# Optimization experiments

Hardware: AMD Instinct MI355X
Metric: run time of the kernel (lower is better)

## Reference

```python
import jax, jax.numpy as jnp
import numpy as np

B, L, D, K, NFFT = 4, 8192, 768, 24, 16384


def setup_inputs() -> dict:
    key = jax.random.key(0)
    k1, k2, k3, k4 = jax.random.split(key, 4)
    x = jax.random.normal(k1, (B, L, D), dtype=jnp.float32)
    phi = jax.random.normal(k2, (L, K), dtype=jnp.float32) * 0.1
    M_inputs = jax.random.normal(k3, (D, D), dtype=jnp.float32) * 0.02
    M_filters = jax.random.normal(k4, (K, D), dtype=jnp.float32) * 0.02
    return {"x": x, "phi": phi, "M_inputs": M_inputs, "M_filters": M_filters, "n": NFFT}


def _convolve_approx(u, v, n):
    # u: (B, L, D) projected inputs; v: (L, D) projected filters (per-channel kernels)
    bsz, seq_len, d = u.shape
    sgn = jnp.where(jnp.arange(seq_len) % 2 == 0, 1.0, -1.0).astype(u.dtype)[None, :, None]  # (1,L,1)
    V = jnp.fft.rfft(v.astype(jnp.float32), n=n, axis=0)[None, :, :, None]  # (1,F,D,1)
    U = jnp.stack([u, u * sgn], axis=-1).astype(jnp.float32)  # (B,L,D,2): [plus, sign-flipped]
    Uf = jnp.fft.rfft(U, n=n, axis=1)  # (B,F,D,2)
    conv = jnp.fft.irfft(V * Uf, n=n, axis=1)[:, :seq_len]  # (B,L,D,2)
    U_plus = conv[..., 0]
    U_minus = conv[..., 1] * sgn
    return U_plus, U_minus


def reference(x, phi, M_inputs, M_filters, n):
    x_proj = x @ M_inputs          # (B,L,D)
    phi_proj = phi @ M_filters     # (L,D)
    spectral_plus, spectral_minus = _convolve_approx(x_proj, phi_proj, n)
    return spectral_plus + spectral_minus
```

## Files before the change

kernel.cpp:

```cpp
#include <hip/hip_runtime.h>
#include <stdint.h>

#define B_SZ 4
#define L_SEQ 8192
#define D_CH 768
#define K_F 24
#define NFFT2 8192
#define LDS_BYTES 69632

typedef __attribute__((ext_vector_type(4))) float f32x4;
typedef __attribute__((ext_vector_type(8))) __bf16 bf16x8;

__device__ __forceinline__ uint32_t f2bf1(float f) {
  uint32_t u = __float_as_uint(f);
  return (u + 0x7fffu + ((u >> 16) & 1u)) >> 16;
}
__device__ __forceinline__ uint32_t packbf2(float lo, float hi) {
  return f2bf1(lo) | (f2bf1(hi) << 16);
}
__device__ __forceinline__ float2 unpackbf2(uint32_t v) {
  return float2{__uint_as_float(v << 16), __uint_as_float(v & 0xffff0000u)};
}
__device__ __forceinline__ float2 cmulf(float2 a, float2 b) {
  return float2{a.x * b.x - a.y * b.y, a.x * b.y + a.y * b.x};
}
__device__ __forceinline__ uint32_t pkbf(float lo, float hi) {
  uint32_t r;
  asm("v_cvt_pk_bf16_f32 %0, %1, %2" : "=v"(r) : "v"(lo), "v"(hi));
  return r;
}

__global__ __launch_bounds__(256) void k_mit(const float* __restrict__ Mi,
                                             uint16_t* __restrict__ MiT) {
  int i = blockIdx.x * 256 + threadIdx.x;
  int n = i / 768, e = i - n * 768;
  MiT[i] = (uint16_t)f2bf1(Mi[e * 768 + n]);
}

template <int S>
__device__ __forceinline__ void dft8(float2* x) {
  const float C = 0.70710678118654752f;
  float2 t0{x[0].x + x[4].x, x[0].y + x[4].y}, t1{x[0].x - x[4].x, x[0].y - x[4].y};
  float2 t2{x[2].x + x[6].x, x[2].y + x[6].y}, t3{x[2].x - x[6].x, x[2].y - x[6].y};
  float2 t4{x[1].x + x[5].x, x[1].y + x[5].y}, t5{x[1].x - x[5].x, x[1].y - x[5].y};
  float2 t6{x[3].x + x[7].x, x[3].y + x[7].y}, t7{x[3].x - x[7].x, x[3].y - x[7].y};
  float2 t3r = (S < 0) ? float2{t3.y, -t3.x} : float2{-t3.y, t3.x};
  float2 t7r = (S < 0) ? float2{t7.y, -t7.x} : float2{-t7.y, t7.x};
  float2 e0{t0.x + t2.x, t0.y + t2.y}, e2{t0.x - t2.x, t0.y - t2.y};
  float2 e1{t1.x + t3r.x, t1.y + t3r.y}, e3{t1.x - t3r.x, t1.y - t3r.y};
  float2 o0{t4.x + t6.x, t4.y + t6.y}, o2{t4.x - t6.x, t4.y - t6.y};
  float2 o1{t5.x + t7r.x, t5.y + t7r.y}, o3{t5.x - t7r.x, t5.y - t7r.y};
  float2 o1r = (S < 0) ? float2{C * (o1.x + o1.y), C * (o1.y - o1.x)}
                       : float2{C * (o1.x - o1.y), C * (o1.y + o1.x)};
  float2 o2r = (S < 0) ? float2{o2.y, -o2.x} : float2{-o2.y, o2.x};
  float2 o3r = (S < 0) ? float2{C * (o3.y - o3.x), -C * (o3.x + o3.y)}
                       : float2{-C * (o3.x + o3.y), C * (o3.x - o3.y)};
  x[0] = float2{e0.x + o0.x, e0.y + o0.y};
  x[4] = float2{e0.x - o0.x, e0.y - o0.y};
  x[1] = float2{e1.x + o1r.x, e1.y + o1r.y};
  x[5] = float2{e1.x - o1r.x, e1.y - o1r.y};
  x[2] = float2{e2.x + o2r.x, e2.y + o2r.y};
  x[6] = float2{e2.x - o2r.x, e2.y - o2r.y};
  x[3] = float2{e3.x + o3r.x, e3.y + o3r.y};
  x[7] = float2{e3.x - o3r.x, e3.y - o3r.y};
}

template <int LH, int S, int NT>
__device__ __forceinline__ void pass_r8(float2* a, int tid) {
  constexpr int h = 1 << LH;
  constexpr int st = h + (h >> 4);
  const float ang = (S < 0 ? -6.2831853071795864769f : 6.2831853071795864769f) / (float)(h * 8);
  __syncthreads();
#pragma unroll
  for (int jj = 0; jj < 1024 / NT; ++jj) {
    int j = jj * NT + tid;
    int pos = j & (h - 1);
    int base = ((j >> LH) << (LH + 3)) + pos;
    float2* p = a + (base + (base >> 4));
    float2 x[8];
#pragma unroll
    for (int q = 0; q < 8; ++q) x[q] = p[q * st];
    float sn, cs;
    __sincosf(ang * (float)pos, &sn, &cs);
    float2 w{cs, sn};
    if constexpr (S < 0) {
      dft8<-1>(x);
      float2 wq = w;
      x[1] = cmulf(x[1], wq);
#pragma unroll
      for (int q = 2; q < 8; ++q) {
        wq = cmulf(wq, w);
        x[q] = cmulf(x[q], wq);
      }
    } else {
      float2 wq = w;
      x[1] = cmulf(x[1], wq);
#pragma unroll
      for (int q = 2; q < 8; ++q) {
        wq = cmulf(wq, w);
        x[q] = cmulf(x[q], wq);
      }
      dft8<1>(x);
    }
#pragma unroll
    for (int q = 0; q < 8; ++q) p[q * st] = x[q];
  }
}

__device__ __forceinline__ void p1_fused(float2* a, const uint32_t* __restrict__ row32, int tid) {
#pragma unroll
  for (int jj = 0; jj < 2; ++jj) {
    int j = jj * 512 + tid;
    float2 x[8];
#pragma unroll
    for (int q = 0; q < 4; ++q) x[q] = unpackbf2(row32[j + q * 1024]);
    x[4] = x[5] = x[6] = x[7] = float2{0.f, 0.f};
    dft8<-1>(x);
    float sn, cs;
    __sincosf(-6.2831853071795864769f / 8192.0f * (float)j, &sn, &cs);
    float2 w{cs, sn}, wq = w;
    x[1] = cmulf(x[1], wq);
#pragma unroll
    for (int q = 2; q < 8; ++q) {
      wq = cmulf(wq, w);
      x[q] = cmulf(x[q], wq);
    }
    float2* p = a + (j + (j >> 4));
#pragma unroll
    for (int q = 0; q < 8; ++q) p[q * 1088] = x[q];
  }
}

__device__ __forceinline__ void mid_fused(float2* a, const uint32_t* __restrict__ wrow, int tid) {
  __syncthreads();
#pragma unroll
  for (int jj = 0; jj < 8; ++jj) {
    int j = jj * 512 + tid;
    float2* p = a + (2 * j + ((2 * j) >> 4));
    float2 u = p[0], v = p[1];
    float2 s{u.x + v.x, u.y + v.y}, dd{u.x - v.x, u.y - v.y};
    uint2 wv = *(const uint2*)(wrow + 2 * j);
    s = cmulf(s, unpackbf2(wv.x));
    dd = cmulf(dd, unpackbf2(wv.y));
    p[0] = float2{s.x + dd.x, s.y + dd.y};
    p[1] = float2{s.x - dd.x, s.y - dd.y};
  }
}

__device__ __forceinline__ void last_fused(float2* a, uint32_t* __restrict__ out32, int tid) {
  __syncthreads();
#pragma unroll
  for (int jj = 0; jj < 2; ++jj) {
    int j = jj * 512 + tid;
    float2* p = a + (j + (j >> 4));
    float2 x[8];
#pragma unroll
    for (int q = 0; q < 8; ++q) x[q] = p[q * 1088];
    float sn, cs;
    __sincosf(6.2831853071795864769f / 8192.0f * (float)j, &sn, &cs);
    float2 w{cs, sn}, wq = w;
    x[1] = cmulf(x[1], wq);
#pragma unroll
    for (int q = 2; q < 8; ++q) {
      wq = cmulf(wq, w);
      x[q] = cmulf(x[q], wq);
    }
    dft8<1>(x);
#pragma unroll
    for (int q = 0; q < 4; ++q) out32[j + q * 1024] = packbf2(x[q].x, x[q].y);
  }
}

__global__ __launch_bounds__(256) void k_phi(const float* __restrict__ phi,
                                             float2* __restrict__ Phi2) {
  extern __shared__ float2 buf[];
  int k = blockIdx.x, tid = threadIdx.x;
  const float scale = 2.0f / 8192.0f;
  for (int r = tid; r < 4096; r += 256) {
    buf[r + (r >> 4)] = float2{phi[(2 * r) * K_F + k] * scale, 0.0f};
    int r2i = r + 4096;
    buf[r2i + (r2i >> 4)] = float2{0.0f, 0.0f};
  }
  pass_r8<10, -1, 256>(buf, tid);
  pass_r8<7, -1, 256>(buf, tid);
  pass_r8<4, -1, 256>(buf, tid);
  pass_r8<1, -1, 256>(buf, tid);
  __syncthreads();
  for (int j = tid; j < 4096; j += 256) {
    float2* p = buf + (2 * j + ((2 * j) >> 4));
    float2 u = p[0], v = p[1];
    p[0] = float2{u.x + v.x, u.y + v.y};
    p[1] = float2{u.x - v.x, u.y - v.y};
  }
  __syncthreads();
  for (int f = tid; f < NFFT2; f += 256) Phi2[k * NFFT2 + f] = buf[f + (f >> 4)];
}

__global__ __launch_bounds__(256) void k_w2(const float2* __restrict__ Phi2,
                                            const float* __restrict__ Mf,
                                            uint32_t* __restrict__ W2) {
  __shared__ float2 p[K_F][256];
  __shared__ float mf[K_F][32];
  int tid = threadIdx.x;
  int fc = blockIdx.x & 31, dc = blockIdx.x >> 5;
  int f0 = fc * 256, d0 = dc * 32;
  for (int i = tid; i < K_F * 256; i += 256) {
    int k = i >> 8, fl = i & 255;
    p[k][fl] = Phi2[k * NFFT2 + f0 + fl];
  }
  for (int i = tid; i < K_F * 32; i += 256) {
    int k = i >> 5, dl = i & 31;
    mf[k][dl] = Mf[k * D_CH + d0 + dl];
  }
  __syncthreads();
  for (int dl = 0; dl < 32; ++dl) {
    float re = 0.f, im = 0.f;
#pragma unroll
    for (int k = 0; k < K_F; ++k) {
      float m = mf[k][dl];
      re += m * p[k][tid].x;
      im += m * p[k][tid].y;
    }
    W2[(size_t)(d0 + dl) * NFFT2 + f0 + tid] = packbf2(re, im);
  }
}

__device__ __forceinline__ void gload_lds16(const void* g, void* l) {
  __builtin_amdgcn_global_load_lds(
      (const __attribute__((address_space(1))) void*)g,
      (__attribute__((address_space(3))) void*)l, 16, 0, 0);
}

__global__ __launch_bounds__(256) void k_gemm(const float* __restrict__ X,
                                              const uint16_t* __restrict__ MiT,
                                              uint16_t* __restrict__ Cp) {
  __shared__ uint16_t As[128 * 64];
  __shared__ uint16_t Bs[128 * 64];
  int tid = threadIdx.x;
  int lane = tid & 63, wid = tid >> 6;
  int bm = blockIdx.x / 6, bn = blockIdx.x % 6;
  int m0 = bm * 128, n0 = bn * 128;
  int wr = wid >> 1, wc = wid & 1;
  int lm = lane & 15, lg = lane >> 4;
  f32x4 acc[4][4] = {};

  for (int kt = 0; kt < 12; ++kt) {
    int k0 = kt * 64;
    __syncthreads();
#pragma unroll
    for (int it = 0; it < 4; ++it) {
      int s = it * 256 + tid;
      int row = s >> 3;
      int cb = ((s & 7) << 4) ^ ((row & 7) << 4);
      gload_lds16(MiT + (size_t)(n0 + row) * 768 + k0 + (cb >> 1),
                  (char*)Bs + (it * 256 + wid * 64) * 16);
    }
#pragma unroll
    for (int it = 0; it < 4; ++it) {
      int s = it * 256 + tid;
      int row = s >> 3, c16 = s & 7;
      const float* src = X + (size_t)(m0 + row) * 768 + k0 + c16 * 8;
      float4 f0 = *(const float4*)src;
      float4 f1 = *(const float4*)(src + 4);
      uint4 o;
      o.x = pkbf(f0.x, f0.y);
      o.y = pkbf(f0.z, f0.w);
      o.z = pkbf(f1.x, f1.y);
      o.w = pkbf(f1.z, f1.w);
      *(uint4*)((char*)As + row * 128 + ((c16 << 4) ^ ((row & 7) << 4))) = o;
    }
    asm volatile("s_waitcnt vmcnt(0)" ::: "memory");
    __syncthreads();
#pragma unroll
    for (int ks = 0; ks < 2; ++ks) {
      int kbyte = (ks * 32 + lg * 8) * 2;
      bf16x8 a[4], b[4];
#pragma unroll
      for (int mi = 0; mi < 4; ++mi) {
        int row = wr * 64 + mi * 16 + lm;
        a[mi] = *(const bf16x8*)((const char*)As + row * 128 + (kbyte ^ ((row & 7) << 4)));
      }
#pragma unroll
      for (int ni = 0; ni < 4; ++ni) {
        int row = wc * 64 + ni * 16 + lm;
        b[ni] = *(const bf16x8*)((const char*)Bs + row * 128 + (kbyte ^ ((row & 7) << 4)));
      }
#pragma unroll
      for (int mi = 0; mi < 4; ++mi)
#pragma unroll
        for (int ni = 0; ni < 4; ++ni)
          acc[mi][ni] = __builtin_amdgcn_mfma_f32_16x16x32_bf16(a[mi], b[ni], acc[mi][ni], 0, 0, 0);
    }
  }
#pragma unroll
  for (int mi = 0; mi < 4; ++mi) {
#pragma unroll
    for (int ni = 0; ni < 4; ++ni) {
      int mg = m0 + wr * 64 + mi * 16 + lg * 4;
      int dd = n0 + wc * 64 + ni * 16 + lm;
      int bb = mg >> 13, t = mg & 8191;
      f32x4 v = acc[mi][ni];
      uint2 o;
      o.x = packbf2(v[0], v[1]);
      o.y = packbf2(v[2], v[3]);
      *(uint2*)(Cp + ((size_t)bb * 768 + dd) * 8192 + t) = o;
    }
  }
}

__global__ __launch_bounds__(512, 4) void k_conv(const uint16_t* __restrict__ xprojT,
                                                 const uint32_t* __restrict__ W2,
                                                 uint16_t* __restrict__ convo) {
  extern __shared__ float2 buf[];
  int tid = threadIdx.x;
  int bd = blockIdx.x;
  int d = bd % 768;
  const uint32_t* row32 = (const uint32_t*)(xprojT + (size_t)bd * 8192);
  p1_fused(buf, row32, tid);
  pass_r8<7, -1, 512>(buf, tid);
  pass_r8<4, -1, 512>(buf, tid);
  pass_r8<1, -1, 512>(buf, tid);
  mid_fused(buf, W2 + (size_t)d * NFFT2, tid);
  pass_r8<1, 1, 512>(buf, tid);
  pass_r8<4, 1, 512>(buf, tid);
  pass_r8<7, 1, 512>(buf, tid);
  last_fused(buf, (uint32_t*)(convo + (size_t)bd * 8192), tid);
}

__global__ __launch_bounds__(256) void k_tr(const uint16_t* __restrict__ convo,
                                            float* __restrict__ out) {
  __shared__ uint16_t tile[64][72];
  int tid = threadIdx.x;
  int bx = blockIdx.x;
  int b = bx / 1536;
  int r = bx - b * 1536;
  int d0 = (r >> 7) << 6;
  int t0 = (r & 127) << 6;
  {
    int rr = tid >> 3;
    int c8 = (tid & 7) << 3;
#pragma unroll
    for (int p = 0; p < 2; ++p) {
      int row = p * 32 + rr;
      uint4 v = *(const uint4*)(convo + ((size_t)(b * 768 + d0 + row)) * 8192 + t0 + c8);
      *(uint4*)&tile[row][c8] = v;
    }
  }
  __syncthreads();
  {
    int c4 = (tid & 15) << 2;
    int tg = tid >> 4;
#pragma unroll
    for (int p = 0; p < 4; ++p) {
      int tt = p * 16 + tg;
      float4 o;
      o.x = __uint_as_float((uint32_t)tile[c4 + 0][tt] << 16);
      o.y = __uint_as_float((uint32_t)tile[c4 + 1][tt] << 16);
      o.z = __uint_as_float((uint32_t)tile[c4 + 2][tt] << 16);
      o.w = __uint_as_float((uint32_t)tile[c4 + 3][tt] << 16);
      *(float4*)(out + ((size_t)b * 8192 + t0 + tt) * 768 + d0 + c4) = o;
    }
  }
}

extern "C" void kernel_launch(void* const* d_in, const int* in_sizes, int n_in,
                              void* d_out, int out_size, void* d_ws, size_t ws_size,
                              hipStream_t stream) {
  const float* x   = (const float*)d_in[0];
  const float* phi = (const float*)d_in[1];
  const float* Mi  = (const float*)d_in[2];
  const float* Mf  = (const float*)d_in[3];
  float* out = (float*)d_out;

  uint16_t* xprojT = (uint16_t*)d_out + 25165824;

  char* ws = (char*)d_ws;
  uint16_t* convo = (uint16_t*)ws;
  uint32_t* W2    = (uint32_t*)(ws + 50331648);
  float2*   Phi2  = (float2*)(ws + 75497472);
  uint16_t* MiT   = (uint16_t*)(ws + 77070336);

  k_mit<<<2304, 256, 0, stream>>>(Mi, MiT);
  k_phi<<<24, 256, LDS_BYTES, stream>>>(phi, Phi2);
  k_w2<<<768, 256, 0, stream>>>(Phi2, Mf, W2);
  k_gemm<<<1536, 256, 0, stream>>>(x, MiT, xprojT);
  k_conv<<<3072, 512, LDS_BYTES, stream>>>(xprojT, W2, convo);
  k_tr<<<6144, 256, 0, stream>>>(convo, out);
}
```

Measured before the change: 253.2 us.

## Double-buffer GEMM LDS tiles and remap block indices across XCDs

The projection GEMM now uses two LDS buffers for the A and B tiles. The next K-slice's global loads (A into registers, B via direct-to-LDS loads) are issued before the MFMA work on the current slice, and A is converted and written after that work. This aims to hide global-load latency behind compute and leaves one barrier per iteration instead of two. The block index is also permuted so that consecutive tiles are spread across XCDs in groups, for better L2 locality. The cost is twice the LDS per block, which may lower occupancy, and the in-loop wait on the async B loads relies only on implicit ordering of the vmcnt counter.

```diff
diff --git a/kernel.cpp b/kernel.cpp
--- a/kernel.cpp
+++ b/kernel.cpp
@@ -234,43 +234,60 @@
 __global__ __launch_bounds__(256) void k_gemm(const float* __restrict__ X,
                                               const uint16_t* __restrict__ MiT,
                                               uint16_t* __restrict__ Cp) {
-  __shared__ uint16_t As[128 * 64];
-  __shared__ uint16_t Bs[128 * 64];
+  __shared__ uint16_t As[2][128 * 64];
+  __shared__ uint16_t Bs[2][128 * 64];
   int tid = threadIdx.x;
   int lane = tid & 63, wid = tid >> 6;
-  int bm = blockIdx.x / 6, bn = blockIdx.x % 6;
+  int p = blockIdx.x;
+  int v = (p & 7) * 192 + (p >> 3);
+  int bm = v / 6, bn = v % 6;
   int m0 = bm * 128, n0 = bn * 128;
   int wr = wid >> 1, wc = wid & 1;
   int lm = lane & 15, lg = lane >> 4;
   f32x4 acc[4][4] = {};
-
+  float4 fa[8];
+
+#define LOAD_A(k0)                                                       \
+  _Pragma("unroll") for (int it = 0; it < 4; ++it) {                     \
+    int s = it * 256 + tid;                                              \
+    int row = s >> 3, c16 = s & 7;                                       \
+    const float* src = X + (size_t)(m0 + row) * 768 + (k0) + c16 * 8;    \
+    fa[2 * it] = *(const float4*)src;                                    \
+    fa[2 * it + 1] = *(const float4*)(src + 4);                          \
+  }
+#define STAGE_B(buf, k0)                                                 \
+  _Pragma("unroll") for (int it = 0; it < 4; ++it) {                     \
+    int s = it * 256 + tid;                                              \
+    int row = s >> 3;                                                    \
+    int cb = ((s & 7) << 4) ^ ((row & 7) << 4);                          \
+    gload_lds16(MiT + (size_t)(n0 + row) * 768 + (k0) + (cb >> 1),       \
+                (char*)Bs[buf] + (it * 256 + wid * 64) * 16);            \
+  }
+#define WRITE_A(buf)                                                     \
+  _Pragma("unroll") for (int it = 0; it < 4; ++it) {                     \
+    int s = it * 256 + tid;                                              \
+    int row = s >> 3, c16 = s & 7;                                       \
+    uint4 o;                                                             \
+    o.x = pkbf(fa[2 * it].x, fa[2 * it].y);                              \
+    o.y = pkbf(fa[2 * it].z, fa[2 * it].w);                              \
+    o.z = pkbf(fa[2 * it + 1].x, fa[2 * it + 1].y);                      \
+    o.w = pkbf(fa[2 * it + 1].z, fa[2 * it + 1].w);                      \
+    *(uint4*)((char*)As[buf] + row * 128 + ((c16 << 4) ^ ((row & 7) << 4))) = o; \
+  }
+
+  LOAD_A(0);
+  STAGE_B(0, 0);
+  WRITE_A(0);
+  asm volatile("s_waitcnt vmcnt(0)" ::: "memory");
+  __syncthreads();
+
+  int cur = 0;
   for (int kt = 0; kt < 12; ++kt) {
-    int k0 = kt * 64;
-    __syncthreads();
-#pragma unroll
-    for (int it = 0; it < 4; ++it) {
-      int s = it * 256 + tid;
-      int row = s >> 3;
-      int cb = ((s & 7) << 4) ^ ((row & 7) << 4);
-      gload_lds16(MiT + (size_t)(n0 + row) * 768 + k0 + (cb >> 1),
-                  (char*)Bs + (it * 256 + wid * 64) * 16);
-    }
-#pragma unroll
-    for (int it = 0; it < 4; ++it) {
-      int s = it * 256 + tid;
-      int row = s >> 3, c16 = s & 7;
-      const float* src = X + (size_t)(m0 + row) * 768 + k0 + c16 * 8;
-      float4 f0 = *(const float4*)src;
-      float4 f1 = *(const float4*)(src + 4);
-      uint4 o;
-      o.x = pkbf(f0.x, f0.y);
-      o.y = pkbf(f0.z, f0.w);
-      o.z = pkbf(f1.x, f1.y);
-      o.w = pkbf(f1.z, f1.w);
-      *(uint4*)((char*)As + row * 128 + ((c16 << 4) ^ ((row & 7) << 4))) = o;
-    }
-    asm volatile("s_waitcnt vmcnt(0)" ::: "memory");
-    __syncthreads();
+    int k0n = (kt + 1) * 64;
+    if (kt < 11) {
+      LOAD_A(k0n);
+      STAGE_B(cur ^ 1, k0n);
+    }
 #pragma unroll
     for (int ks = 0; ks < 2; ++ks) {
       int kbyte = (ks * 32 + lg * 8) * 2;
@@ -278,12 +295,12 @@
 #pragma unroll
       for (int mi = 0; mi < 4; ++mi) {
         int row = wr * 64 + mi * 16 + lm;
-        a[mi] = *(const bf16x8*)((const char*)As + row * 128 + (kbyte ^ ((row & 7) << 4)));
+        a[mi] = *(const bf16x8*)((const char*)As[cur] + row * 128 + (kbyte ^ ((row & 7) << 4)));
       }
 #pragma unroll
       for (int ni = 0; ni < 4; ++ni) {
         int row = wc * 64 + ni * 16 + lm;
-        b[ni] = *(const bf16x8*)((const char*)Bs + row * 128 + (kbyte ^ ((row & 7) << 4)));
+        b[ni] = *(const bf16x8*)((const char*)Bs[cur] + row * 128 + (kbyte ^ ((row & 7) << 4)));
       }
 #pragma unroll
       for (int mi = 0; mi < 4; ++mi)
@@ -291,7 +308,14 @@
         for (int ni = 0; ni < 4; ++ni)
           acc[mi][ni] = __builtin_amdgcn_mfma_f32_16x16x32_bf16(a[mi], b[ni], acc[mi][ni], 0, 0, 0);
     }
-  }
+    if (kt < 11) WRITE_A(cur ^ 1);
+    __syncthreads();
+    cur ^= 1;
+  }
+#undef LOAD_A
+#undef STAGE_B
+#undef WRITE_A
+
 #pragma unroll
   for (int mi = 0; mi < 4; ++mi) {
 #pragma unroll
@@ -299,10 +323,10 @@
       int mg = m0 + wr * 64 + mi * 16 + lg * 4;
       int dd = n0 + wc * 64 + ni * 16 + lm;
       int bb = mg >> 13, t = mg & 8191;
-      f32x4 v = acc[mi][ni];
+      f32x4 vv = acc[mi][ni];
       uint2 o;
-      o.x = packbf2(v[0], v[1]);
-      o.y = packbf2(v[2], v[3]);
+      o.x = packbf2(vv[0], vv[1]);
+      o.y = packbf2(vv[2], vv[3]);
       *(uint2*)(Cp + ((size_t)bb * 768 + dd) * 8192 + t) = o;
     }
   }
```

Measured after the change: 236.5 us. 6.6% less time.
